# Kernel tuning notes

Hardware: AMD Instinct MI355X
Metric: run time of the kernel (lower is better)

## Reference

```python
import jax, jax.numpy as jnp
import numpy as np
from jax import lax

E, DIM, INTER, TOPK, NT = 32, 2048, 1408, 4, 4096
UP = 2 * INTER          # gated activation: interleaved gate/up columns
BLK = 128               # FP8 block-quant tile size
ALPHA, LIMIT, OFFSET = 1.702, 7.0, 1.0  # quick_geglu constants


def setup_inputs() -> dict:
    key = jax.random.key(0)
    ks = jax.random.split(key, 8)
    x = jax.random.normal(ks[0], (NT, DIM), jnp.float32)
    token_mask = jax.random.bernoulli(ks[1], 0.95, (NT,))
    weights = jax.random.uniform(ks[2], (NT, TOPK), jnp.float32)
    indices = jax.random.randint(ks[3], (NT, TOPK), 0, E)
    # frozen FP8 expert weights + block-wise inverse scales (buffers)
    gate_up_w8 = (jax.random.normal(ks[4], (E, DIM, UP), jnp.float32) * 0.05).astype(jnp.float8_e4m3fn)
    down_w8 = (jax.random.normal(ks[5], (E, INTER, DIM), jnp.float32) * 0.05).astype(jnp.float8_e4m3fn)
    gate_up_scale = jax.random.uniform(ks[6], (E, DIM // BLK, UP // BLK), jnp.float32, 0.5, 1.5)
    down_scale = jax.random.uniform(ks[7], (E, INTER // BLK, DIM // BLK), jnp.float32, 0.5, 1.5)
    return dict(x=x, token_mask=token_mask, weights=weights, indices=indices,
                gate_up_w8=gate_up_w8, down_w8=down_w8,
                gate_up_scale=gate_up_scale, down_scale=down_scale)


def _dequant(w8, sinv):
    # block-wise FP8 dequant: w[e, r, c] * sinv[e, r//128, c//128]
    e, r, c = w8.shape
    w = w8.astype(jnp.float32).reshape(e, r // BLK, BLK, c // BLK, BLK)
    return (w * sinv[:, :, None, :, None]).reshape(e, r, c)


def reference(x, token_mask, weights, indices, gate_up_w8, down_w8, gate_up_scale, down_scale):
    nt, topk = indices.shape
    dim = x.shape[1]
    # mask invalid (token_mask=False or out-of-range expert) routing entries
    valid = token_mask[:, None] & (indices >= 0) & (indices < E)
    fvalid = valid.reshape(-1)
    eid = jnp.where(fvalid, indices.reshape(-1), E)  # invalid -> E, sorts last
    tok = jnp.repeat(jnp.arange(nt), topk)
    probs = jnp.where(fvalid, weights.astype(jnp.float32).reshape(-1), 0.0)
    # stable sort by expert id (matches argsort(stable=True) in source)
    order = jnp.argsort(eid, stable=True)
    s_eid, s_tok, s_prob = eid[order], tok[order], probs[order]
    # invalid rows are clamped into the last expert's group; their prob is 0
    # and they scatter to a dummy slot, so they contribute nothing.
    gs = jnp.bincount(jnp.minimum(s_eid, E - 1), length=E).astype(jnp.int32)
    w_gu = _dequant(gate_up_w8, gate_up_scale)   # [E, dim, 2*inter]
    w_d = _dequant(down_w8, down_scale)          # [E, inter, dim]
    h = x[s_tok]                                  # [T, dim] permuted tokens
    o1 = lax.ragged_dot(h, w_gu, gs)              # grouped GEMM 1: [T, 2*inter]
    gate = jnp.minimum(o1[..., ::2], LIMIT)       # interleaved gate/up split
    up = jnp.clip(o1[..., 1::2], -LIMIT, LIMIT)
    inter = gate * jax.nn.sigmoid(ALPHA * gate) * (up + OFFSET) * s_prob[:, None]
    o2 = lax.ragged_dot(inter, w_d, gs)           # grouped GEMM 2: [T, dim]
    dst = jnp.where(s_eid < E, s_tok, nt)         # dummy slot nt for invalid
    out = jnp.zeros((nt + 1, dim), jnp.float32).at[dst].add(o2)
    return out[:nt].astype(x.dtype)
```

## Files before the change

### kernel.cpp

```cpp
#include <hip/hip_runtime.h>
#include <hip/hip_bf16.h>

#define E_ 32
#define DIM_ 2048
#define INTER_ 1408
#define UP_ 2816
#define NT_ 4096
#define NE_ 16384
#define MAXT 96

typedef __attribute__((ext_vector_type(8))) short bf16x8;
typedef __attribute__((ext_vector_type(4))) float f32x4;
typedef unsigned int uint32;
typedef unsigned long long u64t;

struct Meta {
  int gs[E_];
  int offs[E_ + 1];
  int Ttot;
  int ntiles;
  int tile_e[MAXT];
  int tile_r0[MAXT];
};

__device__ __forceinline__ unsigned short bf16_of(float f) {
  union { __hip_bfloat16 b; unsigned short u; } cv;
  cv.b = __float2bfloat16(f);
  return cv.u;
}

__device__ __forceinline__ bool mask_ok(const void* m, int mode, int tok) {
  if (mode) return ((const uint32*)m)[tok] != 0u;
  return ((const unsigned char*)m)[tok] != 0;
}

__global__ __launch_bounds__(256) void k_route(
    const void* __restrict__ tmask, const float* __restrict__ wts,
    const int* __restrict__ idx, Meta* __restrict__ meta,
    int* __restrict__ s_tok, float* __restrict__ s_prob, int* __restrict__ inv) {
  __shared__ unsigned short tc[E_][257];
  __shared__ int offs_s[E_ + 1];
  __shared__ int tot[E_];
  __shared__ int mmode;
  const int t = threadIdx.x;
  if (t == 0) {
    const uint32* w = (const uint32*)tmask;
    bool word_mode = true;
    for (int i = 0; i < 64; ++i) {
      uint32 v = w[i];
      if (!(v <= 1u || v == 0x3F800000u)) { word_mode = false; break; }
    }
    mmode = word_mode ? 1 : 0;
  }
#pragma unroll
  for (int e = 0; e < E_; ++e) tc[e][t] = 0;
  __syncthreads();
  const int base = t * 64;
  for (int i = 0; i < 64; ++i) {
    int ent = base + i;
    int e = idx[ent];
    bool v = mask_ok(tmask, mmode, ent >> 2) && (e >= 0) && (e < E_);
    if (v) tc[e][t] += 1;
  }
  __syncthreads();
  if (t < E_) {
    int run = 0;
    for (int j = 0; j < 256; ++j) {
      int c = tc[t][j]; tc[t][j] = (unsigned short)run; run += c;
    }
    tot[t] = run;
  }
  __syncthreads();
  if (t == 0) {
    int acc = 0, nt = 0;
    for (int e = 0; e < E_; ++e) {
      offs_s[e] = acc;
      meta->offs[e] = acc;
      meta->gs[e] = tot[e];
      for (int r0 = 0; r0 < tot[e]; r0 += 256) {
        meta->tile_e[nt] = e; meta->tile_r0[nt] = r0; ++nt;
      }
      acc += tot[e];
    }
    offs_s[E_] = acc;
    meta->offs[E_] = acc;
    meta->Ttot = acc;
    meta->ntiles = nt;
  }
  __syncthreads();
  for (int i = 0; i < 64; ++i) {
    int ent = base + i;
    int e = idx[ent];
    bool v = mask_ok(tmask, mmode, ent >> 2) && (e >= 0) && (e < E_);
    if (v) {
      int r = tc[e][t]++;
      int pos = offs_s[e] + r;
      s_tok[pos] = ent >> 2;
      s_prob[pos] = wts[ent];
      inv[ent] = pos;
    } else {
      inv[ent] = -1;
    }
  }
}

__global__ __launch_bounds__(256) void k_xcast(const float* __restrict__ x,
                                               unsigned short* __restrict__ xb) {
  const size_t i = ((size_t)blockIdx.x * 256 + threadIdx.x) * 8;
  f32x4 a = *(const f32x4*)(x + i);
  f32x4 b = *(const f32x4*)(x + i + 4);
  uint4 o;
  o.x = (uint32)bf16_of(a.x) | ((uint32)bf16_of(a.y) << 16);
  o.y = (uint32)bf16_of(a.z) | ((uint32)bf16_of(a.w) << 16);
  o.z = (uint32)bf16_of(b.x) | ((uint32)bf16_of(b.y) << 16);
  o.w = (uint32)bf16_of(b.z) | ((uint32)bf16_of(b.w) << 16);
  *(uint4*)(xb + i) = o;
}

template <int KTOT, int NTOT, bool GEGLU, bool GATHER>
__global__ __launch_bounds__(512) void k_gemm(
    const float* __restrict__ Wf, const float* __restrict__ scale,
    const unsigned short* __restrict__ Asrc, const Meta* __restrict__ meta,
    const int* __restrict__ s_tok, const float* __restrict__ s_prob,
    unsigned short* __restrict__ o_bf16, float* __restrict__ o_f32, int staged) {
  constexpr int NX = NTOT / 128;
  constexpr int NKS = KTOT / 64;
  const int NBact = NX * meta->ntiles;
  const int bid = blockIdx.x;
  if (bid >= NBact) return;
  const int q = NBact >> 3, r = NBact & 7;
  const int x = bid & 7, pos = bid >> 3;
  const int wk = ((x < r) ? x * (q + 1) : r * (q + 1) + (x - r) * q) + pos;
  const int tile = wk / NX;
  const int n0 = (wk % NX) * 128;
  const int e = meta->tile_e[tile];
  const int row0 = meta->tile_r0[tile];
  const int off = meta->offs[e];
  const int gsz = meta->gs[e];

  __shared__ unsigned short As[256 * 64];
  __shared__ unsigned short Bs[128 * 64];

  const int tid = threadIdx.x;
  const int lane = tid & 63;
  const int wid = tid >> 6;
  const int wm = wid >> 1;
  const int wn = wid & 1;

  const char* aSrc[4];
  {
    const int rr = lane >> 3, cc = lane & 7;
#pragma unroll
    for (int i = 0; i < 4; ++i) {
      const int grow = row0 + wid * 32 + i * 8 + rr;
      int slot;
      if (GATHER) slot = (grow < gsz) ? s_tok[off + grow] : 0;
      else slot = off + grow;
      const int key = rr ^ ((wid * 4 + i) & 7);
      aSrc[i] = (const char*)Asrc + (size_t)slot * (KTOT * 2) + ((cc ^ key) << 4);
    }
  }

  const int kq = tid >> 5;
  const int kc = kq >> 1;
  const int half = kq & 1;
  const int n4 = (tid & 31) * 4;

  const float* Bbase = Wf + (size_t)e * KTOT * NTOT + n0;
  const float* sbase = scale + (size_t)e * (KTOT / 128) * (NTOT / 128) + (n0 >> 7);

  f32x4 acc[4][4] = {};
  f32x4 v0[4], v1[4];

#define LOAD_B(KS, V)                                                          \
  {                                                                            \
    const float* Bk = Bbase + (size_t)((KS) * 64 + kq * 4) * NTOT + n4;        \
    _Pragma("unroll") for (int i = 0; i < 4; ++i)                              \
      V[i] = *(const f32x4*)(Bk + (size_t)i * NTOT);                           \
  }

#define ISSUE_A(KS)                                                            \
  {                                                                            \
    _Pragma("unroll") for (int i = 0; i < 4; ++i) {                            \
      __builtin_amdgcn_global_load_lds(                                        \
          (const __attribute__((address_space(1))) uint32*)(aSrc[i] + (size_t)(KS) * 128), \
          (__attribute__((address_space(3))) uint32*)(&As[(wid * 32 + i * 8) * 64]), \
          16, 0, 0);                                                           \
    }                                                                          \
  }

#define WRITE_B(KS, V)                                                         \
  {                                                                            \
    const float bscl = sbase[((KS) >> 1) * (NTOT / 128)];                      \
    _Pragma("unroll") for (int j = 0; j < 4; ++j) {                            \
      const int n = n4 + j;                                                    \
      const int key = (n & 7) ^ ((n >> 3) & 7);                                \
      uint32 lo = (uint32)bf16_of(V[0][j] * bscl) | ((uint32)bf16_of(V[1][j] * bscl) << 16); \
      uint32 hi = (uint32)bf16_of(V[2][j] * bscl) | ((uint32)bf16_of(V[3][j] * bscl) << 16); \
      *(u64t*)&Bs[n * 64 + ((kc ^ key) << 3) + half * 4] = (u64t)lo | ((u64t)hi << 32); \
    }                                                                          \
  }

#define MFMA_STEP()                                                            \
  {                                                                            \
    _Pragma("unroll") for (int sub = 0; sub < 2; ++sub) {                      \
      const int c0 = sub * 4 + (lane >> 4);                                    \
      bf16x8 a[4], b[4];                                                       \
      _Pragma("unroll") for (int fI = 0; fI < 4; ++fI) {                       \
        const int ra = wm * 64 + fI * 16 + (lane & 15);                        \
        const int ka = c0 ^ (ra & 7) ^ ((ra >> 3) & 7);                        \
        a[fI] = *(const bf16x8*)&As[ra * 64 + (ka << 3)];                      \
        const int rb = wn * 64 + fI * 16 + (lane & 15);                        \
        const int kb = c0 ^ (rb & 7) ^ ((rb >> 3) & 7);                        \
        b[fI] = *(const bf16x8*)&Bs[rb * 64 + (kb << 3)];                      \
      }                                                                        \
      _Pragma("unroll") for (int fm = 0; fm < 4; ++fm)                         \
        _Pragma("unroll") for (int fn = 0; fn < 4; ++fn)                       \
          acc[fm][fn] = __builtin_amdgcn_mfma_f32_16x16x32_bf16(a[fm], b[fn], acc[fm][fn], 0, 0, 0); \
    }                                                                          \
  }

  LOAD_B(0, v0);
  LOAD_B(1, v1);
  ISSUE_A(0);
  __builtin_amdgcn_sched_barrier(0);
  WRITE_B(0, v0);
  LOAD_B(2, v0);
  asm volatile("s_waitcnt lgkmcnt(0)" ::: "memory");
  asm volatile("s_waitcnt vmcnt(8)" ::: "memory");
  __builtin_amdgcn_s_barrier();

  for (int ks0 = 0; ks0 < NKS; ks0 += 2) {
    MFMA_STEP();
    __builtin_amdgcn_s_barrier();
    ISSUE_A(ks0 + 1);
    __builtin_amdgcn_sched_barrier(0);
    WRITE_B(ks0 + 1, v1);
    if (ks0 + 3 < NKS) LOAD_B(ks0 + 3, v1);
    asm volatile("s_waitcnt lgkmcnt(0)" ::: "memory");
    if (ks0 + 3 < NKS) asm volatile("s_waitcnt vmcnt(8)" ::: "memory");
    else               asm volatile("s_waitcnt vmcnt(0)" ::: "memory");
    __builtin_amdgcn_s_barrier();
    MFMA_STEP();
    if (ks0 + 2 < NKS) {
      __builtin_amdgcn_s_barrier();
      ISSUE_A(ks0 + 2);
      __builtin_amdgcn_sched_barrier(0);
      WRITE_B(ks0 + 2, v0);
      if (ks0 + 4 < NKS) LOAD_B(ks0 + 4, v0);
      asm volatile("s_waitcnt lgkmcnt(0)" ::: "memory");
      if (ks0 + 4 < NKS) asm volatile("s_waitcnt vmcnt(8)" ::: "memory");
      else               asm volatile("s_waitcnt vmcnt(0)" ::: "memory");
      __builtin_amdgcn_s_barrier();
    }
  }
#undef LOAD_B
#undef ISSUE_A
#undef WRITE_B
#undef MFMA_STEP

  const int nbase = n0 + wn * 64;
#pragma unroll
  for (int fm = 0; fm < 4; ++fm) {
#pragma unroll
    for (int r2 = 0; r2 < 4; ++r2) {
      const int rl = row0 + wm * 64 + fm * 16 + (lane >> 4) * 4 + r2;
      const bool ok = rl < gsz;
      const int slot = off + rl;
      if constexpr (GEGLU) {
        const float p = ok ? s_prob[slot] : 0.f;
#pragma unroll
        for (int fn = 0; fn < 4; ++fn) {
          float vv = acc[fm][fn][r2];
          float vp = __shfl_xor(vv, 1, 64);
          float g = (lane & 1) ? vp : vv;
          float u = (lane & 1) ? vv : vp;
          g = fminf(g, 7.f);
          u = fminf(fmaxf(u, -7.f), 7.f);
          const float sig = 1.f / (1.f + __expf(-1.702f * g));
          const float val = g * sig * (u + 1.f) * p;
          if (ok && !(lane & 1)) {
            const int c = (nbase + fn * 16 + (lane & 15)) >> 1;
            o_bf16[(size_t)slot * INTER_ + c] = bf16_of(val);
          }
        }
      } else {
        if (staged) {
          float* orow = o_f32 + (size_t)slot * DIM_;
          if (ok) {
#pragma unroll
            for (int fn = 0; fn < 4; ++fn)
              orow[nbase + fn * 16 + (lane & 15)] = acc[fm][fn][r2];
          }
        } else {
          if (ok) {
            float* orow = o_f32 + (size_t)s_tok[slot] * DIM_;
#pragma unroll
            for (int fn = 0; fn < 4; ++fn)
              atomicAdd(&orow[nbase + fn * 16 + (lane & 15)], acc[fm][fn][r2]);
          }
        }
      }
    }
  }
}

__global__ __launch_bounds__(256) void k_reduce(const float* __restrict__ o2s,
                                                const int* __restrict__ inv,
                                                float* __restrict__ out) {
  const int t = blockIdx.x;
  const int c = threadIdx.x * 8;
  f32x4 s0 = {0.f, 0.f, 0.f, 0.f}, s1 = {0.f, 0.f, 0.f, 0.f};
#pragma unroll
  for (int j = 0; j < 4; ++j) {
    const int sl = inv[t * 4 + j];
    if (sl >= 0) {
      const float* r = o2s + (size_t)sl * DIM_ + c;
      f32x4 a = *(const f32x4*)r;
      f32x4 b = *(const f32x4*)(r + 4);
      s0 += a; s1 += b;
    }
  }
  float* o = out + (size_t)t * DIM_ + c;
  *(f32x4*)o = s0;
  *(f32x4*)(o + 4) = s1;
}

extern "C" void kernel_launch(void* const* d_in, const int* in_sizes, int n_in,
                              void* d_out, int out_size, void* d_ws, size_t ws_size,
                              hipStream_t stream) {
  const float* x = (const float*)d_in[0];
  const void* tmask = d_in[1];
  const float* wts = (const float*)d_in[2];
  const int* idx = (const int*)d_in[3];
  const float* gup_w = (const float*)d_in[4];
  const float* dn_w = (const float*)d_in[5];
  const float* gup_sc = (const float*)d_in[6];
  const float* dn_sc = (const float*)d_in[7];
  float* out = (float*)d_out;
  char* ws = (char*)d_ws;

  const size_t xb_off = 262144;
  const size_t inter_off = xb_off + (size_t)NT_ * DIM_ * 2;
  const size_t o2s_off = inter_off + (size_t)(NE_ + 256) * INTER_ * 2;
  const size_t need = o2s_off;
  const size_t need2 = o2s_off + (size_t)(NE_ + 256) * DIM_ * 4;
  if (ws_size < need) return;
  const int staged = (ws_size >= need2) ? 1 : 0;

  Meta* meta = (Meta*)(ws);
  int* s_tok = (int*)(ws + 4096);
  float* s_prob = (float*)(ws + 4096 + NE_ * 4);
  int* inv = (int*)(ws + 4096 + 2 * NE_ * 4);
  unsigned short* xb = (unsigned short*)(ws + xb_off);
  unsigned short* inter = (unsigned short*)(ws + inter_off);
  float* o2s = (float*)(ws + o2s_off);

  if (!staged)
    (void)hipMemsetAsync(d_out, 0, (size_t)out_size * sizeof(float), stream);
  hipLaunchKernelGGL(k_route, dim3(1), dim3(256), 0, stream, tmask, wts, idx, meta, s_tok, s_prob, inv);
  hipLaunchKernelGGL(k_xcast, dim3(NT_ * DIM_ / 2048), dim3(256), 0, stream, x, xb);
  hipLaunchKernelGGL((k_gemm<DIM_, UP_, true, true>), dim3((UP_ / 128) * MAXT), dim3(512), 0,
                     stream, gup_w, gup_sc, xb, meta, s_tok, s_prob, inter, (float*)nullptr, 0);
  hipLaunchKernelGGL((k_gemm<INTER_, DIM_, false, false>), dim3((DIM_ / 128) * MAXT), dim3(512), 0,
                     stream, dn_w, dn_sc, inter, meta, s_tok, s_prob, (unsigned short*)nullptr,
                     staged ? o2s : out, staged);
  if (staged)
    hipLaunchKernelGGL(k_reduce, dim3(NT_), dim3(256), 0, stream, o2s, inv, out);
}
```

Measured before the change: 763.3 us.

## Double-buffer A tile in LDS so gathers overlap MFMA compute

The A-tile shared memory buffer is doubled so the async global-to-LDS gather for the next K step is issued before the current step's MFMAs instead of after a barrier. This overlaps the A-load latency with compute. The thread-to-B-element mapping is also reshuffled, and the vmcnt waits are tightened from 8 to 4 outstanding loads to match. LDS use per block grows by 32 KB, which may lower occupancy.

```diff
diff --git a/kernel.cpp b/kernel.cpp
--- a/kernel.cpp
+++ b/kernel.cpp
@@ -138,7 +138,7 @@
   const int off = meta->offs[e];
   const int gsz = meta->gs[e];
 
-  __shared__ unsigned short As[256 * 64];
+  __shared__ unsigned short As[2][256 * 64];
   __shared__ unsigned short Bs[128 * 64];
 
   const int tid = threadIdx.x;
@@ -161,30 +161,29 @@
     }
   }
 
-  const int kq = tid >> 5;
-  const int kc = kq >> 1;
-  const int half = kq & 1;
-  const int n4 = (tid & 31) * 4;
+  const int kcB = tid >> 6;
+  const int halfB = tid & 1;
+  const int n4 = ((tid >> 1) & 31) * 4;
 
   const float* Bbase = Wf + (size_t)e * KTOT * NTOT + n0;
   const float* sbase = scale + (size_t)e * (KTOT / 128) * (NTOT / 128) + (n0 >> 7);
 
   f32x4 acc[4][4] = {};
-  f32x4 v0[4], v1[4];
+  f32x4 va[4], vb[4];
 
 #define LOAD_B(KS, V)                                                          \
   {                                                                            \
-    const float* Bk = Bbase + (size_t)((KS) * 64 + kq * 4) * NTOT + n4;        \
+    const float* Bk = Bbase + (size_t)((KS) * 64 + kcB * 8 + halfB * 4) * NTOT + n4; \
     _Pragma("unroll") for (int i = 0; i < 4; ++i)                              \
       V[i] = *(const f32x4*)(Bk + (size_t)i * NTOT);                           \
   }
 
-#define ISSUE_A(KS)                                                            \
+#define ISSUE_A(KS, BUF)                                                       \
   {                                                                            \
     _Pragma("unroll") for (int i = 0; i < 4; ++i) {                            \
       __builtin_amdgcn_global_load_lds(                                        \
           (const __attribute__((address_space(1))) uint32*)(aSrc[i] + (size_t)(KS) * 128), \
-          (__attribute__((address_space(3))) uint32*)(&As[(wid * 32 + i * 8) * 64]), \
+          (__attribute__((address_space(3))) uint32*)(&As[BUF][(wid * 32 + i * 8) * 64]), \
           16, 0, 0);                                                           \
     }                                                                          \
   }
@@ -197,11 +196,11 @@
       const int key = (n & 7) ^ ((n >> 3) & 7);                                \
       uint32 lo = (uint32)bf16_of(V[0][j] * bscl) | ((uint32)bf16_of(V[1][j] * bscl) << 16); \
       uint32 hi = (uint32)bf16_of(V[2][j] * bscl) | ((uint32)bf16_of(V[3][j] * bscl) << 16); \
-      *(u64t*)&Bs[n * 64 + ((kc ^ key) << 3) + half * 4] = (u64t)lo | ((u64t)hi << 32); \
+      *(u64t*)&Bs[n * 64 + ((kcB ^ key) << 3) + halfB * 4] = (u64t)lo | ((u64t)hi << 32); \
     }                                                                          \
   }
 
-#define MFMA_STEP()                                                            \
+#define MFMA_STEP(BUF)                                                         \
   {                                                                            \
     _Pragma("unroll") for (int sub = 0; sub < 2; ++sub) {                      \
       const int c0 = sub * 4 + (lane >> 4);                                    \
@@ -209,7 +208,7 @@
       _Pragma("unroll") for (int fI = 0; fI < 4; ++fI) {                       \
         const int ra = wm * 64 + fI * 16 + (lane & 15);                        \
         const int ka = c0 ^ (ra & 7) ^ ((ra >> 3) & 7);                        \
-        a[fI] = *(const bf16x8*)&As[ra * 64 + (ka << 3)];                      \
+        a[fI] = *(const bf16x8*)&As[BUF][ra * 64 + (ka << 3)];                 \
         const int rb = wn * 64 + fI * 16 + (lane & 15);                        \
         const int kb = c0 ^ (rb & 7) ^ ((rb >> 3) & 7);                        \
         b[fI] = *(const bf16x8*)&Bs[rb * 64 + (kb << 3)];                      \
@@ -220,36 +219,38 @@
     }                                                                          \
   }
 
-  LOAD_B(0, v0);
-  LOAD_B(1, v1);
-  ISSUE_A(0);
+  LOAD_B(0, va);
+  LOAD_B(1, vb);
+  ISSUE_A(0, 0);
   __builtin_amdgcn_sched_barrier(0);
-  WRITE_B(0, v0);
-  LOAD_B(2, v0);
+  WRITE_B(0, va);
+  LOAD_B(2, va);
   asm volatile("s_waitcnt lgkmcnt(0)" ::: "memory");
-  asm volatile("s_waitcnt vmcnt(8)" ::: "memory");
+  asm volatile("s_waitcnt vmcnt(4)" ::: "memory");
   __builtin_amdgcn_s_barrier();
 
   for (int ks0 = 0; ks0 < NKS; ks0 += 2) {
-    MFMA_STEP();
+    ISSUE_A(ks0 + 1, 1);
+    __builtin_amdgcn_sched_barrier(0);
+    MFMA_STEP(0);
     __builtin_amdgcn_s_barrier();
-    ISSUE_A(ks0 + 1);
-    __builtin_amdgcn_sched_barrier(0);
-    WRITE_B(ks0 + 1, v1);
-    if (ks0 + 3 < NKS) LOAD_B(ks0 + 3, v1);
+    WRITE_B(ks0 + 1, vb);
+    if (ks0 + 3 < NKS) LOAD_B(ks0 + 3, vb);
     asm volatile("s_waitcnt lgkmcnt(0)" ::: "memory");
-    if (ks0 + 3 < NKS) asm volatile("s_waitcnt vmcnt(8)" ::: "memory");
+    if (ks0 + 3 < NKS) asm volatile("s_waitcnt vmcnt(4)" ::: "memory");
     else               asm volatile("s_waitcnt vmcnt(0)" ::: "memory");
     __builtin_amdgcn_s_barrier();
-    MFMA_STEP();
+    if (ks0 + 2 < NKS) {
+      ISSUE_A(ks0 + 2, 0);
+      __builtin_amdgcn_sched_barrier(0);
+    }
+    MFMA_STEP(1);
     if (ks0 + 2 < NKS) {
       __builtin_amdgcn_s_barrier();
-      ISSUE_A(ks0 + 2);
-      __builtin_amdgcn_sched_barrier(0);
-      WRITE_B(ks0 + 2, v0);
-      if (ks0 + 4 < NKS) LOAD_B(ks0 + 4, v0);
+      WRITE_B(ks0 + 2, va);
+      if (ks0 + 4 < NKS) LOAD_B(ks0 + 4, va);
       asm volatile("s_waitcnt lgkmcnt(0)" ::: "memory");
-      if (ks0 + 4 < NKS) asm volatile("s_waitcnt vmcnt(8)" ::: "memory");
+      if (ks0 + 4 < NKS) asm volatile("s_waitcnt vmcnt(4)" ::: "memory");
       else               asm volatile("s_waitcnt vmcnt(0)" ::: "memory");
       __builtin_amdgcn_s_barrier();
     }
```

Result: slower. 889.8 us (+16.6%).
